# Performance work log

Hardware: AMD Instinct MI355X
Metric: run time of the kernel (lower is better)

Reference implementation:

```python
import jax, jax.numpy as jnp
import numpy as np

N_NODES = 100000
N_EDGES = 3200000
F_X = 24
F_S = 8
H = 64
F_OUT = 32


def setup_inputs() -> dict:
    key = jax.random.key(0)
    ks = jax.random.split(key, 6)
    x = jax.random.normal(ks[0], (N_NODES, F_X), dtype=jnp.float32)
    scalars = jax.random.normal(ks[1], (F_S,), dtype=jnp.float32)
    edge_index = jax.random.randint(ks[2], (2, N_EDGES), 0, N_NODES, dtype=jnp.int64)
    d_in = F_X + F_S
    W1 = jax.random.normal(ks[3], (d_in, H), dtype=jnp.float32) * (1.0 / np.sqrt(d_in))
    b1 = jnp.zeros((H,), dtype=jnp.float32)
    W2 = jax.random.normal(ks[4], (H, F_OUT), dtype=jnp.float32) * (1.0 / np.sqrt(H))
    b2 = jnp.zeros((F_OUT,), dtype=jnp.float32)
    return {"x": x, "scalars": scalars, "edge_index": edge_index,
            "W1": W1, "b1": b1, "W2": W2, "b2": b2}


def reference(x, scalars, edge_index, W1, b1, W2, b2):
    n = x.shape[0]
    # scalars.view(1,-1).expand(N,-1) then cat along feature dim
    s = jnp.broadcast_to(scalars.reshape(1, -1), (n, scalars.shape[-1]))
    h = jnp.concatenate([x, s], axis=1)  # [N, F_X+F_S]
    src, dst = edge_index[0], edge_index[1]
    # per-edge MLP on gathered source features
    m = h[src]                              # [E, d_in] gather
    m = jax.nn.relu(m @ W1 + b1)            # [E, H]
    m = m @ W2 + b2                         # [E, F_OUT]
    # scatter-add aggregation at destination nodes
    out = jax.ops.segment_sum(m, dst, num_segments=n)  # [N, F_OUT]
    return out
```

## Files before the change

### kernel.cpp

```cpp
#include <hip/hip_runtime.h>

#define N_NODES 100000
#define N_EDGES 3200000
#define F_X 24
#define F_S 8
#define D_IN 32
#define H_DIM 64
#define F_OUT 32

#define NPB 256
#define NBKT 391
#define BCAP 8960
#define P1_THREADS 1024
#define P1_EPT 16
#define P1_EPB (P1_THREADS * P1_EPT)
#define P1_BLOCKS ((N_EDGES + P1_EPB - 1) / P1_EPB)
#define MLP_BLOCKS ((N_NODES + 255) / 256)
#define P2_THREADS 512
#define OFFS_ROW 392

__device__ __forceinline__ unsigned bf16_rne(float f) {
    unsigned u = __float_as_uint(f);
    return (u + 0x7fffu + ((u >> 16) & 1u)) >> 16;
}

__global__ __launch_bounds__(P1_THREADS) void fused_mlp_p1(
    const float* __restrict__ x, const float* __restrict__ scalars,
    const float* __restrict__ W1, const float* __restrict__ b1,
    const float* __restrict__ W2, const float* __restrict__ b2,
    unsigned* __restrict__ y,
    const int* __restrict__ ei,
    unsigned* __restrict__ bbuf,
    int* __restrict__ offs_g)
{
    __shared__ __align__(16) unsigned char smem[68736];
    const int tid = threadIdx.x;

    if (blockIdx.x < P1_BLOCKS) {
        unsigned* sSE  = (unsigned*)smem;
        int* cnt       = (int*)(smem + 65536);
        int* runoff    = (int*)(smem + 67104);
        int* wsum      = (int*)(smem + 68672);

        const int nbase = blockIdx.x * P1_EPB;
        const int nThis = min(P1_EPB, N_EDGES - nbase);

        for (int i = tid; i < NBKT; i += P1_THREADS) cnt[i] = 0;
        __syncthreads();

        unsigned pk[P1_EPT];
        int meta[P1_EPT];
        #pragma unroll
        for (int k = 0; k < P1_EPT; ++k) {
            const int idx = tid + k * P1_THREADS;
            if (idx < nThis) {
                const int e = nbase + idx;
                const int src = ei[e];
                const int dst = ei[N_EDGES + e];
                const int bkt = dst >> 8;
                const int rank = atomicAdd(&cnt[bkt], 1);
                pk[k]   = (unsigned)src | ((unsigned)(dst & 255) << 17);
                meta[k] = bkt | (rank << 9);
            } else {
                meta[k] = -1;
            }
        }
        __syncthreads();

        const int lane = tid & 63, wid = tid >> 6;
        const int cval = (tid < NBKT) ? cnt[tid] : 0;
        int a = cval;
        #pragma unroll
        for (int off = 1; off < 64; off <<= 1) {
            const int u = __shfl_up(a, off, 64);
            if (lane >= off) a += u;
        }
        if (lane == 63) wsum[wid] = a;
        __syncthreads();
        if (tid == 0) {
            int r = 0;
            #pragma unroll
            for (int w = 0; w < 7; ++w) { const int t = wsum[w]; wsum[w] = r; r += t; }
        }
        __syncthreads();
        if (tid <= NBKT) {
            const int bse = wsum[wid] + a - cval;
            runoff[tid] = bse;
            offs_g[blockIdx.x * OFFS_ROW + tid] = bse;
        }
        __syncthreads();

        #pragma unroll
        for (int k = 0; k < P1_EPT; ++k) {
            if (meta[k] >= 0)
                sSE[runoff[meta[k] & 511] + (meta[k] >> 9)] = pk[k];
        }
        __syncthreads();

        const uint4* s4 = (const uint4*)sSE;
        uint4* b4 = (uint4*)(bbuf + (size_t)blockIdx.x * P1_EPB);
        for (int i = tid; i < (nThis >> 2); i += P1_THREADS) b4[i] = s4[i];
    } else {
        float* sW1 = (float*)smem;
        float* sW2 = (float*)(smem + 8192);
        float* sb1 = (float*)(smem + 16384);
        float* sb2 = (float*)(smem + 16640);
        float* ss  = (float*)(smem + 16768);

        for (int i = tid; i < D_IN * H_DIM; i += P1_THREADS) sW1[i] = W1[i];
        for (int i = tid; i < H_DIM * F_OUT; i += P1_THREADS) sW2[i] = W2[i];
        if (tid < H_DIM)  sb1[tid] = b1[tid];
        if (tid < F_OUT)  sb2[tid] = b2[tid];
        if (tid < F_S)    ss[tid]  = scalars[tid];
        __syncthreads();

        const int mb = blockIdx.x - P1_BLOCKS;
        const int v = mb * 256 + (tid >> 2);
        const int c = tid & 3;
        if (v >= N_NODES) return;

        float h[D_IN];
        const float4* xr = reinterpret_cast<const float4*>(x + (size_t)v * F_X);
        #pragma unroll
        for (int i = 0; i < F_X / 4; ++i) {
            float4 t = xr[i];
            h[i * 4 + 0] = t.x; h[i * 4 + 1] = t.y;
            h[i * 4 + 2] = t.z; h[i * 4 + 3] = t.w;
        }
        #pragma unroll
        for (int i = 0; i < F_S; ++i) h[F_X + i] = ss[i];

        float hid[16];
        {
            const float4* bb = reinterpret_cast<const float4*>(sb1 + c * 16);
            #pragma unroll
            for (int q = 0; q < 4; ++q) {
                const float4 t = bb[q];
                hid[q * 4 + 0] = t.x; hid[q * 4 + 1] = t.y;
                hid[q * 4 + 2] = t.z; hid[q * 4 + 3] = t.w;
            }
        }
        #pragma unroll
        for (int k = 0; k < D_IN; ++k) {
            const float hk = h[k];
            const float4* wr = reinterpret_cast<const float4*>(sW1 + k * H_DIM + c * 16);
            #pragma unroll
            for (int q = 0; q < 4; ++q) {
                const float4 t = wr[q];
                hid[q * 4 + 0] = fmaf(hk, t.x, hid[q * 4 + 0]);
                hid[q * 4 + 1] = fmaf(hk, t.y, hid[q * 4 + 1]);
                hid[q * 4 + 2] = fmaf(hk, t.z, hid[q * 4 + 2]);
                hid[q * 4 + 3] = fmaf(hk, t.w, hid[q * 4 + 3]);
            }
        }
        #pragma unroll
        for (int l = 0; l < 16; ++l) hid[l] = fmaxf(hid[l], 0.0f);

        float op[8];
        #pragma unroll
        for (int t = 0; t < 8; ++t) op[t] = 0.0f;

        #pragma unroll
        for (int d = 0; d < 4; ++d) {
            const int cc = c ^ d;
            float ht[16];
            if (d == 0) {
                #pragma unroll
                for (int t = 0; t < 16; ++t) ht[t] = hid[t];
            } else {
                #pragma unroll
                for (int t = 0; t < 16; ++t) ht[t] = __shfl_xor(hid[t], d);
            }
            const int lbase = cc * 16;
            #pragma unroll
            for (int ll = 0; ll < 16; ++ll) {
                const float hl = ht[ll];
                const float4* wr = reinterpret_cast<const float4*>(
                    sW2 + (lbase + ll) * F_OUT + c * 8);
                const float4 t0 = wr[0], t1 = wr[1];
                op[0] = fmaf(hl, t0.x, op[0]);
                op[1] = fmaf(hl, t0.y, op[1]);
                op[2] = fmaf(hl, t0.z, op[2]);
                op[3] = fmaf(hl, t0.w, op[3]);
                op[4] = fmaf(hl, t1.x, op[4]);
                op[5] = fmaf(hl, t1.y, op[5]);
                op[6] = fmaf(hl, t1.z, op[6]);
                op[7] = fmaf(hl, t1.w, op[7]);
            }
        }
        #pragma unroll
        for (int t = 0; t < 8; ++t) op[t] += sb2[c * 8 + t];

        unsigned pk4[4];
        #pragma unroll
        for (int t = 0; t < 4; ++t)
            pk4[t] = bf16_rne(op[2 * t]) | (bf16_rne(op[2 * t + 1]) << 16);
        uint4* yr = reinterpret_cast<uint4*>(y + (size_t)v * 16 + c * 4);
        *yr = make_uint4(pk4[0], pk4[1], pk4[2], pk4[3]);
    }
}

__global__ __launch_bounds__(P2_THREADS) void p2_aggregate(
    const unsigned* __restrict__ bbuf,
    const int* __restrict__ offs_g,
    const unsigned* __restrict__ y,
    float* __restrict__ out)
{
    __shared__ __align__(16) unsigned sE[BCAP];
    __shared__ unsigned sS[BCAP];
    __shared__ int segoff[P1_BLOCKS + 1];
    __shared__ int segsrc[P1_BLOCKS];
    __shared__ int cnt[NPB];
    __shared__ int cur[NPB];
    __shared__ int cbase[NPB + 1];
    __shared__ int wsum8[8];
    __shared__ int wsumT[5];

    const int tid = threadIdx.x;
    const int b = blockIdx.x;
    const int lane = tid & 63, wid = tid >> 6;

    int o0 = 0, cval = 0;
    if (tid < P1_BLOCKS) {
        o0   = offs_g[tid * OFFS_ROW + b];
        cval = offs_g[tid * OFFS_ROW + b + 1] - o0;
        segsrc[tid] = o0;
    }
    int a = cval;
    #pragma unroll
    for (int off = 1; off < 64; off <<= 1) {
        const int u = __shfl_up(a, off, 64);
        if (lane >= off) a += u;
    }
    if (lane == 63) wsum8[wid] = a;
    __syncthreads();
    if (tid == 0) {
        int r = 0;
        #pragma unroll
        for (int w = 0; w < 4; ++w) { const int t = wsum8[w]; wsum8[w] = r; r += t; }
    }
    if (tid < NPB) cnt[tid] = 0;
    __syncthreads();
    if (tid <= P1_BLOCKS) segoff[tid] = wsum8[wid] + a - cval;
    __syncthreads();

    int nE = segoff[P1_BLOCKS];
    if (nE > BCAP) nE = BCAP;

    for (int i = wid; i < P1_BLOCKS; i += P2_THREADS / 64) {
        const int d0 = segoff[i];
        const int cI = segoff[i + 1] - d0;
        const unsigned* g = bbuf + (size_t)i * P1_EPB + segsrc[i];
        for (int j = lane; j < cI; j += 64) {
            const int dp = d0 + j;
            if (dp < BCAP) sE[dp] = g[j];
        }
    }
    __syncthreads();

    for (int i = tid; i < nE; i += P2_THREADS)
        atomicAdd(&cnt[(sE[i] >> 17) & 255u], 1);
    __syncthreads();

    int vcnt = 0, a2 = 0;
    if (tid < NPB) {
        vcnt = cnt[tid];
        a2 = vcnt;
        #pragma unroll
        for (int off = 1; off < 64; off <<= 1) {
            const int u = __shfl_up(a2, off, 64);
            if ((tid & 63) >= off) a2 += u;
        }
        if ((tid & 63) == 63) wsumT[tid >> 6] = a2;
    }
    __syncthreads();
    if (tid == 0) {
        int r = 0;
        #pragma unroll
        for (int w = 0; w < 4; ++w) { const int t = wsumT[w]; wsumT[w] = r; r += t; }
        wsumT[4] = r;
    }
    __syncthreads();
    if (tid < NPB) {
        const int bse = wsumT[tid >> 6] + a2 - vcnt;
        cbase[tid] = bse;
        cur[tid]   = bse;
        if (tid == NPB - 1) cbase[NPB] = wsumT[4];
    }
    __syncthreads();

    for (int i = tid; i < nE; i += P2_THREADS) {
        const unsigned w = sE[i];
        const int pos = atomicAdd(&cur[(w >> 17) & 255u], 1);
        sS[pos] = w & 0x1FFFFu;
    }
    __syncthreads();

    const int g = tid >> 1;
    const int c = tid & 1;
    const int beg = cbase[g];
    const int end = cbase[g + 1];

    float acc[16];
    #pragma unroll
    for (int k = 0; k < 16; ++k) acc[k] = 0.0f;

    int i = beg;
    for (; i + 4 <= end; i += 4) {
        unsigned s[4];
        #pragma unroll
        for (int j = 0; j < 4; ++j) s[j] = sS[i + j];

        uint4 qa[4], qb[4];
        #pragma unroll
        for (int j = 0; j < 4; ++j) {
            const uint4* r = reinterpret_cast<const uint4*>(y + (size_t)s[j] * 16) + 2 * c;
            qa[j] = r[0];
            qb[j] = r[1];
        }
        __builtin_amdgcn_sched_barrier(0);

        #pragma unroll
        for (int j = 0; j < 4; ++j) {
            const unsigned w0[4] = {qa[j].x, qa[j].y, qa[j].z, qa[j].w};
            const unsigned w1[4] = {qb[j].x, qb[j].y, qb[j].z, qb[j].w};
            #pragma unroll
            for (int k = 0; k < 4; ++k) {
                acc[2 * k + 0] += __uint_as_float(w0[k] << 16);
                acc[2 * k + 1] += __uint_as_float(w0[k] & 0xFFFF0000u);
                acc[8 + 2 * k + 0] += __uint_as_float(w1[k] << 16);
                acc[8 + 2 * k + 1] += __uint_as_float(w1[k] & 0xFFFF0000u);
            }
        }
    }
    for (; i < end; ++i) {
        const uint4* r = reinterpret_cast<const uint4*>(y + (size_t)sS[i] * 16) + 2 * c;
        const uint4 qa = r[0], qb = r[1];
        const unsigned w0[4] = {qa.x, qa.y, qa.z, qa.w};
        const unsigned w1[4] = {qb.x, qb.y, qb.z, qb.w};
        #pragma unroll
        for (int k = 0; k < 4; ++k) {
            acc[2 * k + 0] += __uint_as_float(w0[k] << 16);
            acc[2 * k + 1] += __uint_as_float(w0[k] & 0xFFFF0000u);
            acc[8 + 2 * k + 0] += __uint_as_float(w1[k] << 16);
            acc[8 + 2 * k + 1] += __uint_as_float(w1[k] & 0xFFFF0000u);
        }
    }

    const int v = b * NPB + g;
    if (v < N_NODES) {
        float4* op = reinterpret_cast<float4*>(out + (size_t)v * F_OUT + c * 16);
        op[0] = make_float4(acc[0],  acc[1],  acc[2],  acc[3]);
        op[1] = make_float4(acc[4],  acc[5],  acc[6],  acc[7]);
        op[2] = make_float4(acc[8],  acc[9],  acc[10], acc[11]);
        op[3] = make_float4(acc[12], acc[13], acc[14], acc[15]);
    }
}

extern "C" void kernel_launch(void* const* d_in, const int* in_sizes, int n_in,
                              void* d_out, int out_size, void* d_ws, size_t ws_size,
                              hipStream_t stream) {
    const float* x       = (const float*)d_in[0];
    const float* scalars = (const float*)d_in[1];
    const int*   ei      = (const int*)d_in[2];
    const float* W1      = (const float*)d_in[3];
    const float* b1      = (const float*)d_in[4];
    const float* W2      = (const float*)d_in[5];
    const float* b2      = (const float*)d_in[6];
    float* out = (float*)d_out;

    char* ws = (char*)d_ws;
    unsigned* y      = (unsigned*)ws;
    unsigned* bbuf   = (unsigned*)(ws + 6400000);
    int*      offs_g = (int*)(ws + 19245056);

    fused_mlp_p1<<<P1_BLOCKS + MLP_BLOCKS, P1_THREADS, 0, stream>>>(
        x, scalars, W1, b1, W2, b2, y, ei, bbuf, offs_g);

    p2_aggregate<<<NBKT, P2_THREADS, 0, stream>>>(bbuf, offs_g, y, out);
}
```

Baseline: 89.54 us.

## Split aggregation buckets into two half-blocks with four threads per node

The aggregation kernel now launches two blocks per destination bucket. Each block owns 128 nodes and uses four threads per node, each handling 8 output features, in place of two threads handling 16. The staging of all bucket edges into shared memory is removed. Each half-block instead reads the bucket segments from global memory twice, once to count and once to scatter, keeping only the edges that fall in its half. This doubles parallelism and halves shared memory per block, at the cost of each block reading the full bucket's edge stream twice.

```diff
diff --git a/kernel.cpp b/kernel.cpp
--- a/kernel.cpp
+++ b/kernel.cpp
@@ -10,7 +10,6 @@
 
 #define NPB 256
 #define NBKT 391
-#define BCAP 8960
 #define P1_THREADS 1024
 #define P1_EPT 16
 #define P1_EPB (P1_THREADS * P1_EPT)
@@ -18,6 +17,9 @@
 #define MLP_BLOCKS ((N_NODES + 255) / 256)
 #define P2_THREADS 512
 #define OFFS_ROW 392
+
+#define HPB 128
+#define BCAP_H 4608
 
 __device__ __forceinline__ unsigned bf16_rne(float f) {
     unsigned u = __float_as_uint(f);
@@ -206,104 +208,88 @@
     const unsigned* __restrict__ y,
     float* __restrict__ out)
 {
-    __shared__ __align__(16) unsigned sE[BCAP];
-    __shared__ unsigned sS[BCAP];
-    __shared__ int segoff[P1_BLOCKS + 1];
+    __shared__ unsigned sS[BCAP_H];
     __shared__ int segsrc[P1_BLOCKS];
-    __shared__ int cnt[NPB];
-    __shared__ int cur[NPB];
-    __shared__ int cbase[NPB + 1];
-    __shared__ int wsum8[8];
-    __shared__ int wsumT[5];
+    __shared__ int seglen[P1_BLOCKS];
+    __shared__ int cnt[HPB];
+    __shared__ int cur[HPB];
+    __shared__ int cbase[HPB + 1];
+    __shared__ int wsumT[3];
 
     const int tid = threadIdx.x;
-    const int b = blockIdx.x;
+    const int bkt = blockIdx.x >> 1;
+    const int h   = blockIdx.x & 1;
     const int lane = tid & 63, wid = tid >> 6;
 
-    int o0 = 0, cval = 0;
     if (tid < P1_BLOCKS) {
-        o0   = offs_g[tid * OFFS_ROW + b];
-        cval = offs_g[tid * OFFS_ROW + b + 1] - o0;
+        const int o0 = offs_g[tid * OFFS_ROW + bkt];
         segsrc[tid] = o0;
-    }
-    int a = cval;
-    #pragma unroll
-    for (int off = 1; off < 64; off <<= 1) {
-        const int u = __shfl_up(a, off, 64);
-        if (lane >= off) a += u;
-    }
-    if (lane == 63) wsum8[wid] = a;
+        seglen[tid] = offs_g[tid * OFFS_ROW + bkt + 1] - o0;
+    }
+    if (tid < HPB) cnt[tid] = 0;
+    __syncthreads();
+
+    for (int i = wid; i < P1_BLOCKS; i += P2_THREADS / 64) {
+        const int cI = seglen[i];
+        const unsigned* gp = bbuf + (size_t)i * P1_EPB + segsrc[i];
+        for (int j = lane; j < cI; j += 64) {
+            const int dl = (int)((gp[j] >> 17) & 255u);
+            if ((dl >> 7) == h) atomicAdd(&cnt[dl & 127], 1);
+        }
+    }
+    __syncthreads();
+
+    int vcnt = 0, a2 = 0;
+    if (tid < HPB) {
+        vcnt = cnt[tid];
+        a2 = vcnt;
+        #pragma unroll
+        for (int off = 1; off < 64; off <<= 1) {
+            const int u = __shfl_up(a2, off, 64);
+            if (lane >= off) a2 += u;
+        }
+        if (lane == 63) wsumT[tid >> 6] = a2;
+    }
     __syncthreads();
     if (tid == 0) {
         int r = 0;
         #pragma unroll
-        for (int w = 0; w < 4; ++w) { const int t = wsum8[w]; wsum8[w] = r; r += t; }
-    }
-    if (tid < NPB) cnt[tid] = 0;
-    __syncthreads();
-    if (tid <= P1_BLOCKS) segoff[tid] = wsum8[wid] + a - cval;
-    __syncthreads();
-
-    int nE = segoff[P1_BLOCKS];
-    if (nE > BCAP) nE = BCAP;
-
-    for (int i = wid; i < P1_BLOCKS; i += P2_THREADS / 64) {
-        const int d0 = segoff[i];
-        const int cI = segoff[i + 1] - d0;
-        const unsigned* g = bbuf + (size_t)i * P1_EPB + segsrc[i];
-        for (int j = lane; j < cI; j += 64) {
-            const int dp = d0 + j;
-            if (dp < BCAP) sE[dp] = g[j];
-        }
-    }
-    __syncthreads();
-
-    for (int i = tid; i < nE; i += P2_THREADS)
-        atomicAdd(&cnt[(sE[i] >> 17) & 255u], 1);
-    __syncthreads();
-
-    int vcnt = 0, a2 = 0;
-    if (tid < NPB) {
-        vcnt = cnt[tid];
-        a2 = vcnt;
-        #pragma unroll
-        for (int off = 1; off < 64; off <<= 1) {
-            const int u = __shfl_up(a2, off, 64);
-            if ((tid & 63) >= off) a2 += u;
-        }
-        if ((tid & 63) == 63) wsumT[tid >> 6] = a2;
-    }
-    __syncthreads();
-    if (tid == 0) {
-        int r = 0;
-        #pragma unroll
-        for (int w = 0; w < 4; ++w) { const int t = wsumT[w]; wsumT[w] = r; r += t; }
-        wsumT[4] = r;
-    }
-    __syncthreads();
-    if (tid < NPB) {
+        for (int w = 0; w < 2; ++w) { const int t = wsumT[w]; wsumT[w] = r; r += t; }
+        wsumT[2] = r;
+    }
+    __syncthreads();
+    if (tid < HPB) {
         const int bse = wsumT[tid >> 6] + a2 - vcnt;
         cbase[tid] = bse;
         cur[tid]   = bse;
-        if (tid == NPB - 1) cbase[NPB] = wsumT[4];
-    }
-    __syncthreads();
-
-    for (int i = tid; i < nE; i += P2_THREADS) {
-        const unsigned w = sE[i];
-        const int pos = atomicAdd(&cur[(w >> 17) & 255u], 1);
-        sS[pos] = w & 0x1FFFFu;
-    }
-    __syncthreads();
-
-    const int g = tid >> 1;
-    const int c = tid & 1;
-    const int beg = cbase[g];
-    const int end = cbase[g + 1];
-
-    float acc[16];
+        if (tid == HPB - 1) cbase[HPB] = wsumT[2];
+    }
+    __syncthreads();
+
+    for (int i = wid; i < P1_BLOCKS; i += P2_THREADS / 64) {
+        const int cI = seglen[i];
+        const unsigned* gp = bbuf + (size_t)i * P1_EPB + segsrc[i];
+        for (int j = lane; j < cI; j += 64) {
+            const unsigned w = gp[j];
+            const int dl = (int)((w >> 17) & 255u);
+            if ((dl >> 7) == h) {
+                const int pos = atomicAdd(&cur[dl & 127], 1);
+                if (pos < BCAP_H) sS[pos] = w & 0x1FFFFu;
+            }
+        }
+    }
+    __syncthreads();
+
+    const int g = tid >> 2;
+    const int c = tid & 3;
+    int beg = cbase[g];
+    int end = cbase[g + 1];
+    if (end > BCAP_H) end = BCAP_H;
+    if (beg > BCAP_H) beg = BCAP_H;
+
+    float acc[8];
     #pragma unroll
-    for (int k = 0; k < 16; ++k) acc[k] = 0.0f;
+    for (int k = 0; k < 8; ++k) acc[k] = 0.0f;
 
     int i = beg;
     for (; i + 4 <= end; i += 4) {
@@ -311,49 +297,38 @@
         #pragma unroll
         for (int j = 0; j < 4; ++j) s[j] = sS[i + j];
 
-        uint4 qa[4], qb[4];
+        uint4 q[4];
+        #pragma unroll
+        for (int j = 0; j < 4; ++j)
+            q[j] = reinterpret_cast<const uint4*>(y + (size_t)s[j] * 16)[c];
+
+        __builtin_amdgcn_sched_barrier(0);
+
         #pragma unroll
         for (int j = 0; j < 4; ++j) {
-            const uint4* r = reinterpret_cast<const uint4*>(y + (size_t)s[j] * 16) + 2 * c;
-            qa[j] = r[0];
-            qb[j] = r[1];
-        }
-        __builtin_amdgcn_sched_barrier(0);
-
-        #pragma unroll
-        for (int j = 0; j < 4; ++j) {
-            const unsigned w0[4] = {qa[j].x, qa[j].y, qa[j].z, qa[j].w};
-            const unsigned w1[4] = {qb[j].x, qb[j].y, qb[j].z, qb[j].w};
+            const unsigned qq[4] = {q[j].x, q[j].y, q[j].z, q[j].w};
             #pragma unroll
             for (int k = 0; k < 4; ++k) {
-                acc[2 * k + 0] += __uint_as_float(w0[k] << 16);
-                acc[2 * k + 1] += __uint_as_float(w0[k] & 0xFFFF0000u);
-                acc[8 + 2 * k + 0] += __uint_as_float(w1[k] << 16);
-                acc[8 + 2 * k + 1] += __uint_as_float(w1[k] & 0xFFFF0000u);
+                acc[2 * k + 0] += __uint_as_float(qq[k] << 16);
+                acc[2 * k + 1] += __uint_as_float(qq[k] & 0xFFFF0000u);
             }
         }
     }
     for (; i < end; ++i) {
-        const uint4* r = reinterpret_cast<const uint4*>(y + (size_t)sS[i] * 16) + 2 * c;
-        const uint4 qa = r[0], qb = r[1];
-        const unsigned w0[4] = {qa.x, qa.y, qa.z, qa.w};
-        const unsigned w1[4] = {qb.x, qb.y, qb.z, qb.w};
+        const uint4 q = reinterpret_cast<const uint4*>(y + (size_t)sS[i] * 16)[c];
+        const unsigned qq[4] = {q.x, q.y, q.z, q.w};
         #pragma unroll
         for (int k = 0; k < 4; ++k) {
-            acc[2 * k + 0] += __uint_as_float(w0[k] << 16);
-            acc[2 * k + 1] += __uint_as_float(w0[k] & 0xFFFF0000u);
-            acc[8 + 2 * k + 0] += __uint_as_float(w1[k] << 16);
-            acc[8 + 2 * k + 1] += __uint_as_float(w1[k] & 0xFFFF0000u);
-        }
-    }
-
-    const int v = b * NPB + g;
+            acc[2 * k + 0] += __uint_as_float(qq[k] << 16);
+            acc[2 * k + 1] += __uint_as_float(qq[k] & 0xFFFF0000u);
+        }
+    }
+
+    const int v = bkt * NPB + h * HPB + g;
     if (v < N_NODES) {
-        float4* op = reinterpret_cast<float4*>(out + (size_t)v * F_OUT + c * 16);
-        op[0] = make_float4(acc[0],  acc[1],  acc[2],  acc[3]);
-        op[1] = make_float4(acc[4],  acc[5],  acc[6],  acc[7]);
-        op[2] = make_float4(acc[8],  acc[9],  acc[10], acc[11]);
-        op[3] = make_float4(acc[12], acc[13], acc[14], acc[15]);
+        float4* op = reinterpret_cast<float4*>(out + (size_t)v * F_OUT + c * 8);
+        op[0] = make_float4(acc[0], acc[1], acc[2], acc[3]);
+        op[1] = make_float4(acc[4], acc[5], acc[6], acc[7]);
     }
 }
 
@@ -377,5 +352,5 @@
     fused_mlp_p1<<<P1_BLOCKS + MLP_BLOCKS, P1_THREADS, 0, stream>>>(
         x, scalars, W1, b1, W2, b2, y, ei, bbuf, offs_g);
 
-    p2_aggregate<<<NBKT, P2_THREADS, 0, stream>>>(bbuf, offs_g, y, out);
+    p2_aggregate<<<NBKT * 2, P2_THREADS, 0, stream>>>(bbuf, offs_g, y, out);
 }
```

Result: slower. 96.90 us (+8.2%).
